# Kernel optimization log

Hardware: AMD Instinct MI355X
Metric: run time of the kernel (lower is better)

The kernel has to match this reference:

```python
import jax, jax.numpy as jnp
import numpy as np

SIGMA = 0.2
BN_EPS = 1e-5


def setup_inputs() -> dict:
    key = jax.random.key(0)
    k1, k2, k3, k4 = jax.random.split(key, 4)
    B, N, K = 8, 16384, 64
    normals = jax.random.normal(k1, (B, 3, N), dtype=jnp.float32)
    # normalize to unit normals (faithful to what the module consumes in practice)
    normals = normals / jnp.linalg.norm(normals, axis=1, keepdims=True)
    neighbor_idx = jax.random.randint(k2, (B, N, 3), 0, N, dtype=jnp.int64)
    weight_alpha = jax.random.uniform(k3, (1, K, 4), dtype=jnp.float32) * np.pi
    weight_beta = jax.random.uniform(k4, (1, K, 4), dtype=jnp.float32) * (2 * np.pi)
    bn_gamma = jnp.ones((K,), dtype=jnp.float32)
    bn_beta = jnp.zeros((K,), dtype=jnp.float32)
    return {
        "normals": normals,
        "neighbor_idx": neighbor_idx,
        "weight_alpha": weight_alpha,
        "weight_beta": weight_beta,
        "bn_gamma": bn_gamma,
        "bn_beta": bn_beta,
    }


def reference(normals, neighbor_idx, weight_alpha, weight_beta, bn_gamma, bn_beta):
    # normals: (B, 3, N); neighbor_idx: (B, N, 3)
    # kernel directions on unit sphere: W[c, k, m], c in xyz, m in 4 points per kernel
    W = jnp.concatenate(
        [
            jnp.sin(weight_alpha) * jnp.cos(weight_beta),
            jnp.sin(weight_alpha) * jnp.sin(weight_beta),
            jnp.cos(weight_alpha),
        ],
        axis=0,
    )  # (3, K, 4)

    # gather neighbor normals: nbr[b, c, i, j] = normals[b, c, neighbor_idx[b, i, j]]
    nbr = jax.vmap(lambda nm, idx: nm[:, idx])(normals, neighbor_idx)  # (B, 3, N, 3)
    F = jnp.concatenate([normals[:, :, :, None], nbr], axis=3)  # (B, 3, N, 4) face points p

    # squared distances via ||f||^2 + ||w||^2 - 2 f.w  (avoids 6D broadcast of torch code)
    dots = jnp.einsum("bcnp,ckm->bknpm", F, W)  # (B, K, N, 4, 4)
    F2 = jnp.sum(F * F, axis=1)[:, None, :, :, None]  # (B, 1, N, 4, 1)
    W2 = jnp.sum(W * W, axis=0)[None, :, None, None, :]  # (1, K, 1, 1, 4)
    dist = F2 + W2 - 2.0 * dots  # (B, K, N, 4, 4)

    inv = -1.0 / (2.0 * SIGMA * SIGMA)
    feat = jnp.sum(jnp.exp(dist * inv), axis=(3, 4)) / 16.0  # (B, K, N)

    # BatchNorm1d (training mode, biased variance over batch+spatial dims) + ReLU
    mean = jnp.mean(feat, axis=(0, 2), keepdims=True)
    var = jnp.var(feat, axis=(0, 2), keepdims=True)
    xhat = (feat - mean) * jax.lax.rsqrt(var + BN_EPS)
    out = bn_gamma[None, :, None] * xhat + bn_beta[None, :, None]
    return jax.nn.relu(out)
```

## Files before the change

### kernel.cpp

```cpp
#include <hip/hip_runtime.h>

#define BB 8
#define NN 16384
#define KK 64

#if __has_builtin(__builtin_amdgcn_exp2f)
#define EXP2(x) __builtin_amdgcn_exp2f(x)
#else
#define EXP2(x) exp2f(x)
#endif

typedef float v2f __attribute__((ext_vector_type(2)));

#if __has_builtin(__builtin_elementwise_fma)
#define FMA2(a, b, c) __builtin_elementwise_fma((a), (b), (c))
#else
static __device__ inline v2f FMA2(v2f a, v2f b, v2f c) {
    v2f r; r.x = fmaf(a.x, b.x, c.x); r.y = fmaf(a.y, b.y, c.y); return r;
}
#endif

#define LOG2E 1.44269504088896340736f
#define CW (25.0f * LOG2E)
#define CE (-12.5f * LOG2E)

__global__ __launch_bounds__(256) void fkc_prep(
    const float* __restrict__ walpha, const float* __restrict__ wbeta,
    float* __restrict__ wx, float* __restrict__ wy, float* __restrict__ wz)
{
    const int t = threadIdx.x;
    float a = walpha[t];
    float b = wbeta[t];
    float sa = __sinf(a);
    wx[t] = CW * sa * __cosf(b);
    wy[t] = CW * sa * __sinf(b);
    wz[t] = CW * __cosf(a);
}

__global__ __launch_bounds__(256, 8) void fkc_main(
    const float* __restrict__ normals,
    const int*   __restrict__ nidx,
    const float* __restrict__ wx, const float* __restrict__ wy,
    const float* __restrict__ wz,
    float* __restrict__ out,
    float* __restrict__ gsum,
    float* __restrict__ gss)
{
    __shared__ float fl[16][257];
    __shared__ float ps[16][17], pq[16][17];

    const int tid = threadIdx.x;
    const int pg = blockIdx.x >> 2;
    const int k0 = (blockIdx.x & 3) * 16;
    const int gid = pg * 256 + tid;
    const int b = gid >> 14;
    const int n = gid & (NN - 1);
    const float* nb = normals + b * 3 * NN;

    float fx[4], fy[4], fz[4];
    fx[0] = nb[n];
    fy[0] = nb[NN + n];
    fz[0] = nb[2 * NN + n];
    const int ibase = (b * NN + n) * 3;
#pragma unroll
    for (int j = 0; j < 3; ++j) {
        int id = nidx[ibase + j];
        fx[j + 1] = nb[id];
        fy[j + 1] = nb[NN + id];
        fz[j + 1] = nb[2 * NN + id];
    }

    v2f fx01 = {fx[0], fx[1]}, fx23 = {fx[2], fx[3]};
    v2f fy01 = {fy[0], fy[1]}, fy23 = {fy[2], fy[3]};
    v2f fz01 = {fz[0], fz[1]}, fz23 = {fz[2], fz[3]};
    v2f e01, e23;
    {
        v2f n2a = FMA2(fx01, fx01, FMA2(fy01, fy01, fz01 * fz01));
        v2f n2b = FMA2(fx23, fx23, FMA2(fy23, fy23, fz23 * fz23));
        e01 = CE * (n2a + 1.0f);
        e23 = CE * (n2b + 1.0f);
    }

    float* orow = out + (b * KK + k0) * NN + n;
#pragma unroll
    for (int kk = 0; kk < 16; ++kk) {
        v2f acc01 = {0.0f, 0.0f}, acc23 = {0.0f, 0.0f};
#pragma unroll
        for (int m = 0; m < 4; ++m) {
            const int wi = ((k0 + kk) << 2) + m;
            float wxv = wx[wi], wyv = wy[wi], wzv = wz[wi];
            v2f wx2 = {wxv, wxv}, wy2 = {wyv, wyv}, wz2 = {wzv, wzv};
            v2f a01 = FMA2(fz01, wz2, FMA2(fy01, wy2, FMA2(fx01, wx2, e01)));
            v2f a23 = FMA2(fz23, wz2, FMA2(fy23, wy2, FMA2(fx23, wx2, e23)));
            v2f x01 = {EXP2(a01.x), EXP2(a01.y)};
            v2f x23 = {EXP2(a23.x), EXP2(a23.y)};
            acc01 += x01;
            acc23 += x23;
        }
        v2f t2 = acc01 + acc23;
        float acc = t2.x + t2.y;
        orow[kk * NN] = acc;
        fl[kk][tid] = acc;
    }
    __syncthreads();

    {
        const int k = tid & 15;
        const int part = tid >> 4;
        float s = 0.0f, ss = 0.0f;
#pragma unroll
        for (int r = 0; r < 16; ++r) {
            float v = fl[k][part * 16 + r];
            s += v;
            ss = fmaf(v, v, ss);
        }
        ps[k][part] = s;
        pq[k][part] = ss;
    }
    __syncthreads();

    if (tid < 16) {
        float s = 0.0f;
#pragma unroll
        for (int r = 0; r < 16; ++r) s += ps[tid][r];
        atomicAdd(&gsum[k0 + tid], s);
    } else if (tid < 32) {
        const int kk = tid - 16;
        float ss = 0.0f;
#pragma unroll
        for (int r = 0; r < 16; ++r) ss += pq[kk][r];
        atomicAdd(&gss[k0 + kk], ss);
    }
}

__global__ __launch_bounds__(256) void fkc_apply(
    float4* __restrict__ out4,
    const float* __restrict__ gsum,
    const float* __restrict__ gss,
    const float* __restrict__ gamma,
    const float* __restrict__ beta)
{
    const int i = blockIdx.x * 256 + threadIdx.x;
    const int k = (i >> 12) & (KK - 1);

    const float invM = 1.0f / (float)(BB * NN);
    float mean = gsum[k] * invM;
    float var = fmaf(-mean, mean, gss[k] * invM);
    float sc = gamma[k] * rsqrtf(var + 1e-5f);
    float sh = fmaf(-mean, sc, beta[k]);

    float4 v = out4[i];
    v.x = fmaxf(fmaf(v.x, sc, sh), 0.0f);
    v.y = fmaxf(fmaf(v.y, sc, sh), 0.0f);
    v.z = fmaxf(fmaf(v.z, sc, sh), 0.0f);
    v.w = fmaxf(fmaf(v.w, sc, sh), 0.0f);
    out4[i] = v;
}

extern "C" void kernel_launch(void* const* d_in, const int* in_sizes, int n_in,
                              void* d_out, int out_size, void* d_ws, size_t ws_size,
                              hipStream_t stream) {
    const float* normals = (const float*)d_in[0];
    const int*   nidx    = (const int*)d_in[1];
    const float* walpha  = (const float*)d_in[2];
    const float* wbeta   = (const float*)d_in[3];
    const float* gamma   = (const float*)d_in[4];
    const float* beta    = (const float*)d_in[5];
    float* out = (float*)d_out;
    float* ws = (float*)d_ws;

    float* gsum = ws;
    float* gss  = ws + 64;
    float* wxb  = ws + 128;
    float* wyb  = ws + 384;
    float* wzb  = ws + 640;

    hipMemsetAsync(ws, 0, 128 * sizeof(float), stream);

    fkc_prep<<<1, 256, 0, stream>>>(walpha, wbeta, wxb, wyb, wzb);
    fkc_main<<<2048, 256, 0, stream>>>(normals, nidx, wxb, wyb, wzb,
                                       out, gsum, gss);
    fkc_apply<<<8192, 256, 0, stream>>>((float4*)out, gsum, gss, gamma, beta);
}
```

Measured before the change: 110.3 us.

## Fuse BatchNorm apply into main kernel via persistent grid-wide barrier

Replaces the separate statistics and apply kernels with one persistent kernel of 1024 blocks. Each block handles 512 points and keeps its features in shared memory. After atomically accumulating the per-channel sums, every block waits on a global spin barrier, then normalizes and applies ReLU before a single store to global memory. This removes the extra full read and write pass over the 32 MB output and the memset launch, at the cost of a spin barrier that relies on all blocks being co-resident, which is checked through an occupancy query with a fallback path. The BN epsilon is also rescaled to match the un-divided-by-16 feature sums.

```diff
diff --git a/kernel.cpp b/kernel.cpp
--- a/kernel.cpp
+++ b/kernel.cpp
@@ -3,6 +3,7 @@
 #define BB 8
 #define NN 16384
 #define KK 64
+#define GRID_FUSED 1024
 
 #if __has_builtin(__builtin_amdgcn_exp2f)
 #define EXP2(x) __builtin_amdgcn_exp2f(x)
@@ -23,12 +24,17 @@
 #define LOG2E 1.44269504088896340736f
 #define CW (25.0f * LOG2E)
 #define CE (-12.5f * LOG2E)
+#define BN_EPS_SCALED 2.56e-3f
 
 __global__ __launch_bounds__(256) void fkc_prep(
     const float* __restrict__ walpha, const float* __restrict__ wbeta,
-    float* __restrict__ wx, float* __restrict__ wy, float* __restrict__ wz)
+    float* __restrict__ wx, float* __restrict__ wy, float* __restrict__ wz,
+    float* __restrict__ gsum, float* __restrict__ gss,
+    unsigned* __restrict__ bar)
 {
     const int t = threadIdx.x;
+    if (t < 64) { gsum[t] = 0.0f; gss[t] = 0.0f; }
+    if (t == 64) { *bar = 0u; }
     float a = walpha[t];
     float b = wbeta[t];
     float sa = __sinf(a);
@@ -37,14 +43,151 @@
     wz[t] = CW * __cosf(a);
 }
 
-__global__ __launch_bounds__(256, 8) void fkc_main(
+__global__ __launch_bounds__(256, 4) void fkc_fused(
     const float* __restrict__ normals,
     const int*   __restrict__ nidx,
     const float* __restrict__ wx, const float* __restrict__ wy,
     const float* __restrict__ wz,
     float* __restrict__ out,
     float* __restrict__ gsum,
-    float* __restrict__ gss)
+    float* __restrict__ gss,
+    const float* __restrict__ gamma,
+    const float* __restrict__ beta,
+    unsigned* __restrict__ bar)
+{
+    __shared__ float fl[16][513];
+    __shared__ float ps[16][17], pq[16][17];
+    __shared__ float scs[16], shs[16];
+
+    const int tid = threadIdx.x;
+    const int pg2 = blockIdx.x >> 2;
+    const int k0 = (blockIdx.x & 3) * 16;
+    const int gid0 = pg2 * 512 + tid;
+    const int b = gid0 >> 14;
+    const int n0 = gid0 & (NN - 1);
+    const float* nb = normals + b * 3 * NN;
+
+#pragma unroll
+    for (int h = 0; h < 2; ++h) {
+        const int n = n0 + h * 256;
+        float fx[4], fy[4], fz[4];
+        fx[0] = nb[n];
+        fy[0] = nb[NN + n];
+        fz[0] = nb[2 * NN + n];
+        const int ibase = (b * NN + n) * 3;
+#pragma unroll
+        for (int j = 0; j < 3; ++j) {
+            int id = nidx[ibase + j];
+            fx[j + 1] = nb[id];
+            fy[j + 1] = nb[NN + id];
+            fz[j + 1] = nb[2 * NN + id];
+        }
+
+        v2f fx01 = {fx[0], fx[1]}, fx23 = {fx[2], fx[3]};
+        v2f fy01 = {fy[0], fy[1]}, fy23 = {fy[2], fy[3]};
+        v2f fz01 = {fz[0], fz[1]}, fz23 = {fz[2], fz[3]};
+        v2f e01, e23;
+        {
+            v2f n2a = FMA2(fx01, fx01, FMA2(fy01, fy01, fz01 * fz01));
+            v2f n2b = FMA2(fx23, fx23, FMA2(fy23, fy23, fz23 * fz23));
+            e01 = CE * (n2a + 1.0f);
+            e23 = CE * (n2b + 1.0f);
+        }
+
+#pragma unroll
+        for (int kk = 0; kk < 16; ++kk) {
+            v2f acc01 = {0.0f, 0.0f}, acc23 = {0.0f, 0.0f};
+#pragma unroll
+            for (int m = 0; m < 4; ++m) {
+                const int wi = ((k0 + kk) << 2) + m;
+                float wxv = wx[wi], wyv = wy[wi], wzv = wz[wi];
+                v2f wx2 = {wxv, wxv}, wy2 = {wyv, wyv}, wz2 = {wzv, wzv};
+                v2f a01 = FMA2(fz01, wz2, FMA2(fy01, wy2, FMA2(fx01, wx2, e01)));
+                v2f a23 = FMA2(fz23, wz2, FMA2(fy23, wy2, FMA2(fx23, wx2, e23)));
+                v2f x01 = {EXP2(a01.x), EXP2(a01.y)};
+                v2f x23 = {EXP2(a23.x), EXP2(a23.y)};
+                acc01 += x01;
+                acc23 += x23;
+            }
+            v2f t2 = acc01 + acc23;
+            fl[kk][h * 256 + tid] = t2.x + t2.y;
+        }
+    }
+    __syncthreads();
+
+    {
+        const int k = tid & 15;
+        const int part = tid >> 4;
+        float s = 0.0f, ss = 0.0f;
+#pragma unroll
+        for (int r = 0; r < 16; ++r) {
+            float v = fl[k][part * 16 + r];
+            s += v;
+            ss = fmaf(v, v, ss);
+            float w = fl[k][256 + part * 16 + r];
+            s += w;
+            ss = fmaf(w, w, ss);
+        }
+        ps[k][part] = s;
+        pq[k][part] = ss;
+    }
+    __syncthreads();
+
+    if (tid < 16) {
+        float s = 0.0f;
+#pragma unroll
+        for (int r = 0; r < 16; ++r) s += ps[tid][r];
+        atomicAdd(&gsum[k0 + tid], s);
+    } else if (tid < 32) {
+        const int kk = tid - 16;
+        float ss = 0.0f;
+#pragma unroll
+        for (int r = 0; r < 16; ++r) ss += pq[kk][r];
+        atomicAdd(&gss[k0 + kk], ss);
+    }
+
+    __syncthreads();
+    if (tid == 0) {
+        __hip_atomic_fetch_add(bar, 1u, __ATOMIC_ACQ_REL,
+                               __HIP_MEMORY_SCOPE_AGENT);
+        int polls = 0;
+        while (__hip_atomic_load(bar, __ATOMIC_ACQUIRE,
+                                 __HIP_MEMORY_SCOPE_AGENT) < GRID_FUSED) {
+            __builtin_amdgcn_s_sleep(16);
+            if (++polls > 200000) break;
+        }
+    }
+    __syncthreads();
+
+    if (tid < 16) {
+        const float invM = 1.0f / (float)(BB * NN);
+        float s = __hip_atomic_load(&gsum[k0 + tid], __ATOMIC_RELAXED,
+                                    __HIP_MEMORY_SCOPE_AGENT);
+        float q = __hip_atomic_load(&gss[k0 + tid], __ATOMIC_RELAXED,
+                                    __HIP_MEMORY_SCOPE_AGENT);
+        float mean = s * invM;
+        float var = fmaf(-mean, mean, q * invM);
+        float sc = gamma[k0 + tid] * rsqrtf(var + BN_EPS_SCALED);
+        scs[tid] = sc;
+        shs[tid] = fmaf(-mean, sc, beta[k0 + tid]);
+    }
+    __syncthreads();
+
+    float* orow = out + (b * KK + k0) * NN + n0;
+#pragma unroll
+    for (int kk = 0; kk < 16; ++kk) {
+        float va = fmaxf(fmaf(fl[kk][tid], scs[kk], shs[kk]), 0.0f);
+        float vb = fmaxf(fmaf(fl[kk][256 + tid], scs[kk], shs[kk]), 0.0f);
+        orow[kk * NN] = va;
+        orow[kk * NN + 256] = vb;
+    }
+}
+
+__global__ __launch_bounds__(256, 8) void fkc_main(
+    const float* __restrict__ normals, const int* __restrict__ nidx,
+    const float* __restrict__ wx, const float* __restrict__ wy,
+    const float* __restrict__ wz,
+    float* __restrict__ out, float* __restrict__ gsum, float* __restrict__ gss)
 {
     __shared__ float fl[16][257];
     __shared__ float ps[16][17], pq[16][17];
@@ -135,10 +278,8 @@
 
 __global__ __launch_bounds__(256) void fkc_apply(
     float4* __restrict__ out4,
-    const float* __restrict__ gsum,
-    const float* __restrict__ gss,
-    const float* __restrict__ gamma,
-    const float* __restrict__ beta)
+    const float* __restrict__ gsum, const float* __restrict__ gss,
+    const float* __restrict__ gamma, const float* __restrict__ beta)
 {
     const int i = blockIdx.x * 256 + threadIdx.x;
     const int k = (i >> 12) & (KK - 1);
@@ -146,7 +287,7 @@
     const float invM = 1.0f / (float)(BB * NN);
     float mean = gsum[k] * invM;
     float var = fmaf(-mean, mean, gss[k] * invM);
-    float sc = gamma[k] * rsqrtf(var + 1e-5f);
+    float sc = gamma[k] * rsqrtf(var + BN_EPS_SCALED);
     float sh = fmaf(-mean, sc, beta[k]);
 
     float4 v = out4[i];
@@ -169,16 +310,34 @@
     float* out = (float*)d_out;
     float* ws = (float*)d_ws;
 
-    float* gsum = ws;
-    float* gss  = ws + 64;
-    float* wxb  = ws + 128;
-    float* wyb  = ws + 384;
-    float* wzb  = ws + 640;
-
-    hipMemsetAsync(ws, 0, 128 * sizeof(float), stream);
-
-    fkc_prep<<<1, 256, 0, stream>>>(walpha, wbeta, wxb, wyb, wzb);
-    fkc_main<<<2048, 256, 0, stream>>>(normals, nidx, wxb, wyb, wzb,
-                                       out, gsum, gss);
-    fkc_apply<<<8192, 256, 0, stream>>>((float4*)out, gsum, gss, gamma, beta);
-}
+    float* gsum   = ws;
+    float* gss    = ws + 64;
+    unsigned* bar = (unsigned*)(ws + 128);
+    float* wxb    = ws + 192;
+    float* wyb    = ws + 448;
+    float* wzb    = ws + 704;
+
+    static int use_fused = -1;
+    if (use_fused < 0) {
+        int occ = 0, ncu = 0, dev = 0;
+        hipError_t e1 = hipOccupancyMaxActiveBlocksPerMultiprocessor(
+            &occ, fkc_fused, 256, 0);
+        hipGetDevice(&dev);
+        hipError_t e2 = hipDeviceGetAttribute(
+            &ncu, hipDeviceAttributeMultiprocessorCount, dev);
+        use_fused = (e1 == hipSuccess && e2 == hipSuccess &&
+                     (long)occ * ncu >= GRID_FUSED) ? 1 : 0;
+    }
+
+    fkc_prep<<<1, 256, 0, stream>>>(walpha, wbeta, wxb, wyb, wzb,
+                                    gsum, gss, bar);
+    if (use_fused) {
+        fkc_fused<<<GRID_FUSED, 256, 0, stream>>>(
+            normals, nidx, wxb, wyb, wzb, out, gsum, gss, gamma, beta, bar);
+    } else {
+        fkc_main<<<2048, 256, 0, stream>>>(normals, nidx, wxb, wyb, wzb,
+                                           out, gsum, gss);
+        fkc_apply<<<8192, 256, 0, stream>>>((float4*)out, gsum, gss,
+                                            gamma, beta);
+    }
+}
```

Result: slower. 204.6 us (+85.4%).
